# Optimization experiments

Measured on AMD Instinct MI355X. Metric: run time of the kernel, lower is better.

## Reference

```python
import jax, jax.numpy as jnp
import numpy as np
from jax import lax

B, T, C, H, HOR = 64, 2048, 64, 256, 96
BETA, THR = 0.9, 1.0


def setup_inputs() -> dict:
    key = jax.random.key(0)
    ks = jax.random.split(key, 10)
    s = lambda *sh: 1.0 / np.sqrt(sh[-1])
    return {
        "x": jax.random.normal(ks[0], (B, T, C), jnp.float32),
        "snn_w": jax.random.uniform(ks[1], (H, C), jnp.float32, -s(C), s(C)),
        "snn_b": jax.random.uniform(ks[2], (H,), jnp.float32, -s(C), s(C)),
        "gru_wih": jax.random.uniform(ks[3], (3 * H, C + H), jnp.float32, -s(H), s(H)),
        "gru_whh": jax.random.uniform(ks[4], (3 * H, H), jnp.float32, -s(H), s(H)),
        "gru_bih": jax.random.uniform(ks[5], (3 * H,), jnp.float32, -s(H), s(H)),
        "gru_bhh": jax.random.uniform(ks[6], (3 * H,), jnp.float32, -s(H), s(H)),
        "head_w": jax.random.uniform(ks[7], (HOR, H), jnp.float32, -s(H), s(H)),
        "head_b": jax.random.uniform(ks[8], (HOR,), jnp.float32, -s(H), s(H)),
    }


@jax.custom_vjp
def spike(x):
    return (x > 0).astype(x.dtype)

def _spike_fwd(x):
    return spike(x), x

def _spike_bwd(x, g):
    # snntorch ATan surrogate, alpha=2: grad = 1 / (1 + (pi*x)^2)
    return (g / (1.0 + (jnp.pi * x) ** 2),)

spike.defvjp(_spike_fwd, _spike_bwd)


def reference(x, snn_w, snn_b, gru_wih, gru_whh, gru_bih, gru_bhh, head_w, head_b):
    # Batched SNN input current across all timesteps: [B,T,H]
    cur = jnp.einsum("btc,hc->bth", x, snn_w) + snn_b

    def lif_step(mem, i_t):
        # reset computed from previous mem, detached (snntorch mem_reset)
        reset = lax.stop_gradient((mem > THR).astype(mem.dtype))
        mem_new = BETA * mem + i_t - reset * THR
        spk = spike(mem_new - THR)
        return mem_new, spk

    mem0 = jnp.zeros((B, H), x.dtype)
    _, spks = lax.scan(lif_step, mem0, cur.transpose(1, 0, 2))  # [T,B,H]

    h_comb = jnp.concatenate([x, spks.transpose(1, 0, 2)], axis=-1)  # [B,T,C+H]

    # GRU: precompute input gates for all timesteps
    gx = jnp.einsum("btc,gc->btg", h_comb, gru_wih) + gru_bih  # [B,T,3H]

    def gru_step(h, gx_t):
        gh = h @ gru_whh.T + gru_bhh
        xr, xz, xn = jnp.split(gx_t, 3, axis=-1)
        hr, hz, hn = jnp.split(gh, 3, axis=-1)
        r = jax.nn.sigmoid(xr + hr)
        z = jax.nn.sigmoid(xz + hz)
        n = jnp.tanh(xn + r * hn)
        h_new = (1.0 - z) * n + z * h
        return h_new, None

    h0 = jnp.zeros((B, H), x.dtype)
    hT, _ = lax.scan(gru_step, h0, gx.transpose(1, 0, 2))

    return hT @ head_w.T + head_b  # [B, HOR]
```

## Files before the change

kernel.cpp:

```cpp
#include <hip/hip_runtime.h>
#include <cstdint>
#include <cstddef>

#define B_   64
#define T_   2048
#define C_   64
#define H_   256
#define G3_  768
#define HOR_ 96

typedef _Float16 h2 __attribute__((ext_vector_type(2)));
typedef _Float16 h8 __attribute__((ext_vector_type(8)));
typedef _Float16 f16x8 __attribute__((ext_vector_type(8)));
typedef float f32x4 __attribute__((ext_vector_type(4)));

#define K1_TT 128
__global__ __launch_bounds__(256) void k_cur(const float* __restrict__ x,
                                             const float* __restrict__ w,
                                             const float* __restrict__ bias,
                                             float* __restrict__ cur,
                                             int* __restrict__ flags) {
  __shared__ float xs[K1_TT * C_];
  const int b = blockIdx.x;
  const int t0 = blockIdx.y * K1_TT;
  const int tid = threadIdx.x;

  if (b == 0 && blockIdx.y == 0) {
#pragma unroll
    for (int i = 0; i < 4; i++) flags[tid + i * 256] = 0;
  }

  const float4* xsrc = (const float4*)(x + ((size_t)b * T_ + t0) * C_);
  float4* xdst = (float4*)xs;
#pragma unroll
  for (int i = 0; i < (K1_TT * C_ / 4) / 256; i++)
    xdst[tid + i * 256] = xsrc[tid + i * 256];

  float wr[C_];
  const float4* wp = (const float4*)(w + (size_t)tid * C_);
#pragma unroll
  for (int q = 0; q < C_ / 4; q++) {
    float4 v = wp[q];
    wr[4 * q + 0] = v.x; wr[4 * q + 1] = v.y;
    wr[4 * q + 2] = v.z; wr[4 * q + 3] = v.w;
  }
  const float bb = bias[tid];
  __syncthreads();

  for (int t = 0; t < K1_TT; t++) {
    const float4* xrow = (const float4*)(xs + t * C_);
    float a0 = 0.f, a1 = 0.f;
#pragma unroll
    for (int q = 0; q < C_ / 4; q += 2) {
      float4 v0 = xrow[q];
      float4 v1 = xrow[q + 1];
      a0 += wr[4 * q + 0] * v0.x + wr[4 * q + 1] * v0.y +
            wr[4 * q + 2] * v0.z + wr[4 * q + 3] * v0.w;
      a1 += wr[4 * q + 4] * v1.x + wr[4 * q + 5] * v1.y +
            wr[4 * q + 6] * v1.z + wr[4 * q + 7] * v1.w;
    }
    cur[((size_t)b * T_ + t0 + t) * H_ + tid] = a0 + a1 + bb;
  }
}

__global__ __launch_bounds__(64) void k_lif(const float* __restrict__ cur,
                                            unsigned char* __restrict__ spk) {
  const int b = blockIdx.x >> 2;
  const int h = ((blockIdx.x & 3) << 6) + threadIdx.x;
  const float* cp = cur + (size_t)b * T_ * H_ + h;
  unsigned char* sp = spk + (size_t)b * T_ * H_ + h;
  float mem = 0.f;
#pragma unroll 32
  for (int t = 0; t < T_; t++) {
    float c = cp[(size_t)t * H_];
    float reset = (mem > 1.0f) ? 1.0f : 0.0f;
    mem = 0.9f * mem + c - reset;
    sp[(size_t)t * H_] = (mem > 1.0f) ? (unsigned char)1 : (unsigned char)0;
  }
}

#define GM 128
#define GN 128
#define AKP 40
#define CTP 136
#define DQ_ (0.0625f / (127.0f * 127.0f))
__global__ __launch_bounds__(256) void k_fused(
    const float* __restrict__ x, const unsigned char* __restrict__ spk,
    const float* __restrict__ wih, const float* __restrict__ bih,
    _Float16* __restrict__ gx, const float* __restrict__ whh,
    const float* __restrict__ bhh, const float* __restrict__ head_w,
    const float* __restrict__ head_b, float* __restrict__ out,
    int* __restrict__ flags) {
  alignas(16) __shared__ _Float16 Ah[GM * AKP];
  alignas(16) __shared__ _Float16 Bh[GN * AKP];
  alignas(16) __shared__ _Float16 Ct[GM * CTP];
  alignas(16) __shared__ int hq[2][64];
  __shared__ float hbuf32[H_];

  const int tid = threadIdx.x;
  const int lane = tid & 63;

  if (blockIdx.x >= 64) {
    const int pidx = blockIdx.x - 64;
    const int bb = pidx / 3;
    const int pp = pidx - bb * 3;
    const int wave = tid >> 6;
    const int ln = lane & 15;
    const int qd = lane >> 4;
    const int wm = (wave & 1) * 64;
    const int wn = ((wave >> 1) & 1) * 64;

    for (int mt = 0; mt < 16; mt++) {
      const int m0 = bb * 2048 + mt * 128;
      for (int nh = 0; nh < 2; nh++) {
        const int n0 = pp * 256 + nh * 128;
        f32x4 acc[4][4] = {};
        for (int kc = 0; kc < 10; kc++) {
          const int k0 = kc * 32;
          if (k0 < 64) {
#pragma unroll
            for (int i = 0; i < 4; i++) {
              int idx = tid + i * 256;
              int r = idx >> 3;
              int c4 = (idx & 7) * 4;
              float4 v = *(const float4*)(x + (size_t)(m0 + r) * C_ + k0 + c4);
              h2 lo, hi;
              lo.x = (_Float16)v.x; lo.y = (_Float16)v.y;
              hi.x = (_Float16)v.z; hi.y = (_Float16)v.w;
              h2* d = (h2*)&Ah[r * AKP + c4];
              d[0] = lo; d[1] = hi;
            }
          } else {
#pragma unroll
            for (int i = 0; i < 4; i++) {
              int idx = tid + i * 256;
              int r = idx >> 3;
              int c4 = (idx & 7) * 4;
              uchar4 u = *(const uchar4*)(spk + (size_t)(m0 + r) * H_ + (k0 - 64) + c4);
              h2 lo, hi;
              lo.x = (_Float16)(int)u.x; lo.y = (_Float16)(int)u.y;
              hi.x = (_Float16)(int)u.z; hi.y = (_Float16)(int)u.w;
              h2* d = (h2*)&Ah[r * AKP + c4];
              d[0] = lo; d[1] = hi;
            }
          }
#pragma unroll
          for (int i = 0; i < 4; i++) {
            int idx = tid + i * 256;
            int r = idx >> 3;
            int c4 = (idx & 7) * 4;
            float4 v = *(const float4*)(wih + (size_t)(n0 + r) * 320 + k0 + c4);
            h2 lo, hi;
            lo.x = (_Float16)v.x; lo.y = (_Float16)v.y;
            hi.x = (_Float16)v.z; hi.y = (_Float16)v.w;
            h2* d = (h2*)&Bh[r * AKP + c4];
            d[0] = lo; d[1] = hi;
          }
          __syncthreads();
          {
            f16x8 a[4], bbf[4];
#pragma unroll
            for (int mtl = 0; mtl < 4; mtl++)
              a[mtl] = *(const f16x8*)&Ah[(wm + mtl * 16 + ln) * AKP + qd * 8];
#pragma unroll
            for (int nt = 0; nt < 4; nt++)
              bbf[nt] = *(const f16x8*)&Bh[(wn + nt * 16 + ln) * AKP + qd * 8];
#pragma unroll
            for (int mtl = 0; mtl < 4; mtl++)
#pragma unroll
              for (int nt = 0; nt < 4; nt++)
                acc[mtl][nt] = __builtin_amdgcn_mfma_f32_16x16x32_f16(
                    a[mtl], bbf[nt], acc[mtl][nt], 0, 0, 0);
          }
          __syncthreads();
        }
        {
          float bias[4];
#pragma unroll
          for (int nt = 0; nt < 4; nt++) bias[nt] = bih[n0 + wn + nt * 16 + ln];
#pragma unroll
          for (int mtl = 0; mtl < 4; mtl++)
#pragma unroll
            for (int nt = 0; nt < 4; nt++) {
              int n = wn + nt * 16 + ln;
#pragma unroll
              for (int r = 0; r < 4; r++) {
                int m = wm + mtl * 16 + qd * 4 + r;
                Ct[m * CTP + n] = (_Float16)(acc[mtl][nt][r] + bias[nt]);
              }
            }
        }
        __syncthreads();
#pragma unroll
        for (int i = 0; i < 8; i++) {
          int idx = tid + i * 256;
          int r = idx >> 4;
          int c = (idx & 15) * 8;
          *(h8*)(gx + (size_t)(m0 + r) * G3_ + n0 + c) = *(const h8*)&Ct[r * CTP + c];
        }
        __syncthreads();
      }
      if (tid == 0)
        __hip_atomic_fetch_add(&flags[bb * 16 + mt], 1, __ATOMIC_RELEASE,
                               __HIP_MEMORY_SCOPE_AGENT);
    }
    return;
  }

  const int b = blockIdx.x;
  const int j = tid;

  int wr[64], wz[64], wn[64];
  {
    const float qs = 2032.0f;
    const float4* p0 = (const float4*)(whh + (size_t)j * H_);
    const float4* p1 = (const float4*)(whh + (size_t)(H_ + j) * H_);
    const float4* p2 = (const float4*)(whh + (size_t)(2 * H_ + j) * H_);
#pragma unroll
    for (int q = 0; q < 64; q++) {
      float4 a = p0[q];
      wr[q] = ((int)rintf(a.x * qs) & 255) | (((int)rintf(a.y * qs) & 255) << 8) |
              (((int)rintf(a.z * qs) & 255) << 16) | (((int)rintf(a.w * qs) & 255) << 24);
      float4 c = p1[q];
      wz[q] = ((int)rintf(c.x * qs) & 255) | (((int)rintf(c.y * qs) & 255) << 8) |
              (((int)rintf(c.z * qs) & 255) << 16) | (((int)rintf(c.w * qs) & 255) << 24);
      float4 d = p2[q];
      wn[q] = ((int)rintf(d.x * qs) & 255) | (((int)rintf(d.y * qs) & 255) << 8) |
              (((int)rintf(d.z * qs) & 255) << 16) | (((int)rintf(d.w * qs) & 255) << 24);
    }
  }
  const float br_ = bhh[j], bz_ = bhh[H_ + j], bn_ = bhh[2 * H_ + j];

  if (tid < 128) ((int*)hq)[tid] = 0;
  float hj = 0.f;
  __syncthreads();

  const _Float16* gxb = gx + (size_t)b * T_ * G3_;
  int p = 0;
  for (int mt = 0; mt < 16; mt++) {
    if (tid == 0) {
      while (__hip_atomic_load(&flags[b * 16 + mt], __ATOMIC_ACQUIRE,
                               __HIP_MEMORY_SCOPE_AGENT) < 3)
        __builtin_amdgcn_s_sleep(8);
    }
    __syncthreads();

    const _Float16* gc = gxb + (size_t)mt * 128 * G3_;
    _Float16 pr = gc[j], pz = gc[H_ + j], pn = gc[2 * H_ + j];

    for (int tt = 0; tt < 128; tt++) {
      float xr = (float)pr, xz = (float)pz, xn = (float)pn;
      if (tt < 127) {
        const _Float16* g = gc + (size_t)(tt + 1) * G3_;
        pr = g[j]; pz = g[H_ + j]; pn = g[2 * H_ + j];
      }

      const int* hb = hq[p];
      int ar0 = 0, ar1 = 0, az0 = 0, az1 = 0, an0 = 0, an1 = 0;
#pragma unroll
      for (int g4 = 0; g4 < 4; g4++) {
#pragma unroll
        for (int cc = 0; cc < 4; cc++) {
          int c = g4 * 4 + cc;
          int4 hv = *(const int4*)(hb + c * 4);
#pragma unroll
          for (int i = 0; i < 4; i++) {
            int h4 = (i == 0) ? hv.x : (i == 1) ? hv.y : (i == 2) ? hv.z : hv.w;
            int wi = c * 4 + i;
            if (wi & 1) {
              ar1 = __builtin_amdgcn_sdot4(wr[wi], h4, ar1, false);
              az1 = __builtin_amdgcn_sdot4(wz[wi], h4, az1, false);
              an1 = __builtin_amdgcn_sdot4(wn[wi], h4, an1, false);
            } else {
              ar0 = __builtin_amdgcn_sdot4(wr[wi], h4, ar0, false);
              az0 = __builtin_amdgcn_sdot4(wz[wi], h4, az0, false);
              an0 = __builtin_amdgcn_sdot4(wn[wi], h4, an0, false);
            }
          }
        }
        __builtin_amdgcn_sched_barrier(2 | 4 | 16 | 32 | 64);
      }
      int ar = ar0 + ar1, az = az0 + az1, an = an0 + an1;

      float r = 1.f / (1.f + __expf(-(xr + (float)ar * DQ_ + br_)));
      float z = 1.f / (1.f + __expf(-(xz + (float)az * DQ_ + bz_)));
      float pre = xn + r * ((float)an * DQ_ + bn_);
      float e = __expf(2.f * pre);
      float n = 1.f - 2.f / (e + 1.f);
      hj = (1.f - z) * n + z * hj;

      ((char*)hq[p ^ 1])[j] = (char)(int)rintf(hj * 127.0f);
      p ^= 1;
      __syncthreads();
    }
  }

  hbuf32[j] = hj;
  __syncthreads();

  if (tid < HOR_) {
    const float4* hw = (const float4*)(head_w + (size_t)tid * H_);
    const float4* hv4 = (const float4*)hbuf32;
    float acc = head_b[tid];
#pragma unroll
    for (int q = 0; q < H_ / 4; q++) {
      float4 w4 = hw[q];
      float4 v4 = hv4[q];
      acc += w4.x * v4.x + w4.y * v4.y + w4.z * v4.z + w4.w * v4.w;
    }
    out[(size_t)b * HOR_ + tid] = acc;
  }
}

extern "C" void kernel_launch(void* const* d_in, const int* in_sizes, int n_in,
                              void* d_out, int out_size, void* d_ws, size_t ws_size,
                              hipStream_t stream) {
  const float* x      = (const float*)d_in[0];
  const float* snn_w  = (const float*)d_in[1];
  const float* snn_b  = (const float*)d_in[2];
  const float* wih    = (const float*)d_in[3];
  const float* whh    = (const float*)d_in[4];
  const float* bih    = (const float*)d_in[5];
  const float* bhh    = (const float*)d_in[6];
  const float* head_w = (const float*)d_in[7];
  const float* head_b = (const float*)d_in[8];
  float* out = (float*)d_out;

  char* ws = (char*)d_ws;
  _Float16* gx = (_Float16*)ws;
  float* cur = (float*)ws;
  unsigned char* spk = (unsigned char*)(ws + (size_t)201326592);
  int* flags = (int*)(ws + (size_t)234881024);

  k_cur<<<dim3(B_, T_ / K1_TT), 256, 0, stream>>>(x, snn_w, snn_b, cur, flags);
  k_lif<<<dim3(256), 64, 0, stream>>>(cur, spk);
  k_fused<<<dim3(256), 256, 0, stream>>>(x, spk, wih, bih, gx, whh, bhh,
                                         head_w, head_b, out, flags);
}
```

Baseline: 1.852 ms.

## Fuse SNN current and LIF scan into gx producer blocks with spike flags

Removes the separate k_cur and k_lif kernels. The pp==0 producer block for each batch now computes the SNN input current from staged x tiles and runs the LIF recurrence in registers, writing spikes directly. It then signals a per-tile spike flag that the pp==1 and pp==2 blocks wait on before their gx GEMM. This drops the large fp32 cur round trip through global memory and lets the spike computation overlap with the GRU pipeline. The cost is extra serial work in one producer block per batch and added inter-block waiting, which could delay gx readiness for the GRU consumer.

```diff
diff --git a/kernel.cpp b/kernel.cpp
--- a/kernel.cpp
+++ b/kernel.cpp
@@ -14,69 +14,9 @@
 typedef _Float16 f16x8 __attribute__((ext_vector_type(8)));
 typedef float f32x4 __attribute__((ext_vector_type(4)));
 
-#define K1_TT 128
-__global__ __launch_bounds__(256) void k_cur(const float* __restrict__ x,
-                                             const float* __restrict__ w,
-                                             const float* __restrict__ bias,
-                                             float* __restrict__ cur,
-                                             int* __restrict__ flags) {
-  __shared__ float xs[K1_TT * C_];
-  const int b = blockIdx.x;
-  const int t0 = blockIdx.y * K1_TT;
-  const int tid = threadIdx.x;
-
-  if (b == 0 && blockIdx.y == 0) {
-#pragma unroll
-    for (int i = 0; i < 4; i++) flags[tid + i * 256] = 0;
-  }
-
-  const float4* xsrc = (const float4*)(x + ((size_t)b * T_ + t0) * C_);
-  float4* xdst = (float4*)xs;
-#pragma unroll
-  for (int i = 0; i < (K1_TT * C_ / 4) / 256; i++)
-    xdst[tid + i * 256] = xsrc[tid + i * 256];
-
-  float wr[C_];
-  const float4* wp = (const float4*)(w + (size_t)tid * C_);
-#pragma unroll
-  for (int q = 0; q < C_ / 4; q++) {
-    float4 v = wp[q];
-    wr[4 * q + 0] = v.x; wr[4 * q + 1] = v.y;
-    wr[4 * q + 2] = v.z; wr[4 * q + 3] = v.w;
-  }
-  const float bb = bias[tid];
-  __syncthreads();
-
-  for (int t = 0; t < K1_TT; t++) {
-    const float4* xrow = (const float4*)(xs + t * C_);
-    float a0 = 0.f, a1 = 0.f;
-#pragma unroll
-    for (int q = 0; q < C_ / 4; q += 2) {
-      float4 v0 = xrow[q];
-      float4 v1 = xrow[q + 1];
-      a0 += wr[4 * q + 0] * v0.x + wr[4 * q + 1] * v0.y +
-            wr[4 * q + 2] * v0.z + wr[4 * q + 3] * v0.w;
-      a1 += wr[4 * q + 4] * v1.x + wr[4 * q + 5] * v1.y +
-            wr[4 * q + 6] * v1.z + wr[4 * q + 7] * v1.w;
-    }
-    cur[((size_t)b * T_ + t0 + t) * H_ + tid] = a0 + a1 + bb;
-  }
-}
-
-__global__ __launch_bounds__(64) void k_lif(const float* __restrict__ cur,
-                                            unsigned char* __restrict__ spk) {
-  const int b = blockIdx.x >> 2;
-  const int h = ((blockIdx.x & 3) << 6) + threadIdx.x;
-  const float* cp = cur + (size_t)b * T_ * H_ + h;
-  unsigned char* sp = spk + (size_t)b * T_ * H_ + h;
-  float mem = 0.f;
-#pragma unroll 32
-  for (int t = 0; t < T_; t++) {
-    float c = cp[(size_t)t * H_];
-    float reset = (mem > 1.0f) ? 1.0f : 0.0f;
-    mem = 0.9f * mem + c - reset;
-    sp[(size_t)t * H_] = (mem > 1.0f) ? (unsigned char)1 : (unsigned char)0;
-  }
+__global__ void k_zero(int* __restrict__ flags) {
+  flags[threadIdx.x] = 0;
+  flags[threadIdx.x + 1024] = 0;
 }
 
 #define GM 128
@@ -85,12 +25,13 @@
 #define CTP 136
 #define DQ_ (0.0625f / (127.0f * 127.0f))
 __global__ __launch_bounds__(256) void k_fused(
-    const float* __restrict__ x, const unsigned char* __restrict__ spk,
+    const float* __restrict__ x, unsigned char* __restrict__ spk,
     const float* __restrict__ wih, const float* __restrict__ bih,
     _Float16* __restrict__ gx, const float* __restrict__ whh,
     const float* __restrict__ bhh, const float* __restrict__ head_w,
     const float* __restrict__ head_b, float* __restrict__ out,
-    int* __restrict__ flags) {
+    const float* __restrict__ snn_w, const float* __restrict__ snn_b,
+    int* __restrict__ gxf, int* __restrict__ spkf) {
   alignas(16) __shared__ _Float16 Ah[GM * AKP];
   alignas(16) __shared__ _Float16 Bh[GN * AKP];
   alignas(16) __shared__ _Float16 Ct[GM * CTP];
@@ -110,8 +51,73 @@
     const int wm = (wave & 1) * 64;
     const int wn = ((wave >> 1) & 1) * 64;
 
+    float snw[C_];
+    float snb = 0.f, mem = 0.f;
+    if (pp == 0) {
+      const float4* wp = (const float4*)(snn_w + (size_t)tid * C_);
+#pragma unroll
+      for (int q = 0; q < C_ / 4; q++) {
+        float4 v = wp[q];
+        snw[4 * q + 0] = v.x; snw[4 * q + 1] = v.y;
+        snw[4 * q + 2] = v.z; snw[4 * q + 3] = v.w;
+      }
+      snb = snn_b[tid];
+    }
+
     for (int mt = 0; mt < 16; mt++) {
-      const int m0 = bb * 2048 + mt * 128;
+      const int t0g = bb * 2048 + mt * 128;
+
+      if (pp == 0) {
+        float* xstage = (float*)Ah;
+        for (int s = 0; s < 4; s++) {
+          __syncthreads();
+#pragma unroll
+          for (int i = 0; i < 2; i++) {
+            int idx = tid + i * 256;
+            int r = idx >> 4;
+            int c4 = (idx & 15) * 4;
+            *(float4*)&xstage[r * C_ + c4] =
+                *(const float4*)(x + (size_t)(t0g + s * 32 + r) * C_ + c4);
+          }
+          __syncthreads();
+          float curv[32];
+#pragma unroll
+          for (int t = 0; t < 32; t++) {
+            const float4* xrow = (const float4*)(xstage + t * C_);
+            float a0 = 0.f, a1 = 0.f;
+#pragma unroll
+            for (int q = 0; q < C_ / 4; q += 2) {
+              float4 v0 = xrow[q];
+              float4 v1 = xrow[q + 1];
+              a0 += snw[4 * q + 0] * v0.x + snw[4 * q + 1] * v0.y +
+                    snw[4 * q + 2] * v0.z + snw[4 * q + 3] * v0.w;
+              a1 += snw[4 * q + 4] * v1.x + snw[4 * q + 5] * v1.y +
+                    snw[4 * q + 6] * v1.z + snw[4 * q + 7] * v1.w;
+            }
+            curv[t] = a0 + a1 + snb;
+          }
+          unsigned char* spb = spk + (size_t)(t0g + s * 32) * H_ + tid;
+#pragma unroll
+          for (int t = 0; t < 32; t++) {
+            float reset = (mem > 1.0f) ? 1.0f : 0.0f;
+            mem = 0.9f * mem + curv[t] - reset;
+            spb[(size_t)t * H_] = (mem > 1.0f) ? (unsigned char)1 : (unsigned char)0;
+          }
+        }
+        __syncthreads();
+        if (tid == 0)
+          __hip_atomic_fetch_add(&spkf[bb * 16 + mt], 1, __ATOMIC_RELEASE,
+                                 __HIP_MEMORY_SCOPE_AGENT);
+      } else {
+        if (tid == 0) {
+          while (__hip_atomic_load(&spkf[bb * 16 + mt], __ATOMIC_ACQUIRE,
+                                   __HIP_MEMORY_SCOPE_AGENT) < 1)
+            __builtin_amdgcn_s_sleep(8);
+        }
+        __syncthreads();
+      }
+
+      const int m0 = t0g;
       for (int nh = 0; nh < 2; nh++) {
         const int n0 = pp * 256 + nh * 128;
         f32x4 acc[4][4] = {};
@@ -201,7 +207,7 @@
         __syncthreads();
       }
       if (tid == 0)
-        __hip_atomic_fetch_add(&flags[bb * 16 + mt], 1, __ATOMIC_RELEASE,
+        __hip_atomic_fetch_add(&gxf[bb * 16 + mt], 1, __ATOMIC_RELEASE,
                                __HIP_MEMORY_SCOPE_AGENT);
     }
     return;
@@ -239,7 +245,7 @@
   int p = 0;
   for (int mt = 0; mt < 16; mt++) {
     if (tid == 0) {
-      while (__hip_atomic_load(&flags[b * 16 + mt], __ATOMIC_ACQUIRE,
+      while (__hip_atomic_load(&gxf[b * 16 + mt], __ATOMIC_ACQUIRE,
                                __HIP_MEMORY_SCOPE_AGENT) < 3)
         __builtin_amdgcn_s_sleep(8);
     }
@@ -328,12 +334,12 @@
 
   char* ws = (char*)d_ws;
   _Float16* gx = (_Float16*)ws;
-  float* cur = (float*)ws;
   unsigned char* spk = (unsigned char*)(ws + (size_t)201326592);
-  int* flags = (int*)(ws + (size_t)234881024);
-
-  k_cur<<<dim3(B_, T_ / K1_TT), 256, 0, stream>>>(x, snn_w, snn_b, cur, flags);
-  k_lif<<<dim3(256), 64, 0, stream>>>(cur, spk);
+  int* gxf  = (int*)(ws + (size_t)234881024);
+  int* spkf = (int*)(ws + (size_t)234885120);
+
+  k_zero<<<1, 1024, 0, stream>>>(gxf);
   k_fused<<<dim3(256), 256, 0, stream>>>(x, spk, wih, bih, gx, whh, bhh,
-                                         head_w, head_b, out, flags);
+                                         head_w, head_b, out, snn_w, snn_b,
+                                         gxf, spkf);
 }
```

After: 2.019 ms. +9.0%, slower.
